# Kernel optimization log

Measured on AMD Instinct MI355X. Metric: run time of the kernel, lower is better.

The kernel has to match this reference:

```python
import jax, jax.numpy as jnp
import numpy as np

HIDDEN = 2048
N_HEADS = 32
HEAD_DIM = HIDDEN // N_HEADS  # 64
SEQ = 2048
BATCH = 1
CHUNK = 256
TOPK = 4
THETA = 10000.0
EPS = 1e-6
NEG = jnp.float32(-1e30)


def setup_inputs() -> dict:
    key = jax.random.key(0)
    ks = jax.random.split(key, 8)
    s = 0.02
    return {
        "hidden_states": jax.random.normal(ks[0], (BATCH, SEQ, HIDDEN), jnp.float32),
        "Wq": jax.random.normal(ks[1], (HIDDEN, HIDDEN), jnp.float32) * s,
        "Wk": jax.random.normal(ks[2], (HIDDEN, HIDDEN), jnp.float32) * s,
        "Wv": jax.random.normal(ks[3], (HIDDEN, HIDDEN), jnp.float32) * s,
        "Wo": jax.random.normal(ks[4], (HIDDEN, HIDDEN), jnp.float32) * s,
        "Wg1": jax.random.normal(ks[5], (HEAD_DIM, HIDDEN), jnp.float32) * s,
        "Wg2": jax.random.normal(ks[6], (HIDDEN, HEAD_DIM), jnp.float32) * s,
        "o_norm_weight": jnp.ones((HEAD_DIM,), jnp.float32),
    }


def _rope(t):
    # t: [B, S, H, D]; non-interleaved (NeoX-style) rotary over full head dim
    D = t.shape[-1]
    pos = jnp.arange(t.shape[1], dtype=jnp.float32)
    inv_freq = 1.0 / (THETA ** (jnp.arange(0, D, 2, dtype=jnp.float32) / D))
    freqs = pos[:, None] * inv_freq[None, :]            # [S, D/2]
    cos = jnp.cos(freqs)[None, :, None, :]
    sin = jnp.sin(freqs)[None, :, None, :]
    t1, t2 = t[..., : D // 2], t[..., D // 2:]
    return jnp.concatenate([t1 * cos - t2 * sin, t1 * sin + t2 * cos], axis=-1)


def reference(hidden_states, Wq, Wk, Wv, Wo, Wg1, Wg2, o_norm_weight):
    B, S, _ = hidden_states.shape
    H, D, C = N_HEADS, HEAD_DIM, CHUNK
    NC = S // C

    q = (hidden_states @ Wq.T).reshape(B, S, H, D)
    k = (hidden_states @ Wk.T).reshape(B, S, H, D)
    v = (hidden_states @ Wv.T).reshape(B, S, H, D)
    q, k = _rope(q), _rope(k)

    # --- MoBA gating: per-chunk mean-pooled keys scored against each query ---
    kmean = k.reshape(B, NC, C, H, D).mean(axis=2)           # [B, NC, H, D]
    gate = jnp.einsum('bshd,bnhd->bhsn', q, kmean)           # [B, H, S, NC]

    pos = jnp.arange(S)
    q_chunk = pos // C                                       # [S]
    chunk_ids = jnp.arange(NC)
    future = chunk_ids[None, :] > q_chunk[:, None]           # [S, NC]
    self_blk = chunk_ids[None, :] == q_chunk[:, None]
    gate = jnp.where(future[None, None], NEG, gate)
    gate = jnp.where(self_blk[None, None], -NEG, gate)       # self block always selected

    _, topk_idx = jax.lax.top_k(gate, TOPK)                  # [B, H, S, TOPK]
    sel = jax.nn.one_hot(topk_idx, NC, dtype=jnp.bool_).any(axis=-2)  # [B, H, S, NC]

    # --- block-sparse causal attention over selected chunks ---
    allowed = jnp.take(sel, q_chunk, axis=-1)                # [B, H, S, S] key j -> chunk j//C
    causal = pos[None, :] <= pos[:, None]                    # [S, S]
    allowed = allowed & causal[None, None]

    scale = 1.0 / np.sqrt(D)
    scores = jnp.einsum('bshd,bthd->bhst', q, k) * scale
    scores = jnp.where(allowed, scores, NEG)
    p = jax.nn.softmax(scores, axis=-1)
    o = jnp.einsum('bhst,bthd->bshd', p, v)                  # [B, S, H, D]

    # --- gated RMSNorm (FusedRMSNormGated, sigmoid activation) ---
    g = ((hidden_states @ Wg1.T) @ Wg2.T).reshape(B, S, H, D)
    rms = jax.lax.rsqrt(jnp.mean(o * o, axis=-1, keepdims=True) + EPS)
    o = o * rms * o_norm_weight * jax.nn.sigmoid(g)

    return (o.reshape(B, S, H * D)) @ Wo.T
```

## Files before the change

kernel.cpp:

```cpp
#include <hip/hip_runtime.h>
#include <hip/hip_bf16.h>


typedef __attribute__((ext_vector_type(8))) short s8v;
typedef __attribute__((ext_vector_type(4))) float f4v;

#define MFMA16(A,B,C) __builtin_amdgcn_mfma_f32_16x16x32_bf16(A,B,C,0,0,0)

__device__ __forceinline__ unsigned short f2b_rne(float f){
  unsigned u = __builtin_bit_cast(unsigned, f);
  u = (u + 0x7FFFu + ((u>>16)&1u)) >> 16;
  return (unsigned short)u;
}
__device__ __forceinline__ float b2f(unsigned short h){
  unsigned u = ((unsigned)h)<<16;
  return __builtin_bit_cast(float, u);
}
__device__ __forceinline__ unsigned pack2(float a, float b){
  return (unsigned)f2b_rne(a) | ((unsigned)f2b_rne(b)<<16);
}
__device__ __forceinline__ void gld16(const void* g, void* l){
  __builtin_amdgcn_global_load_lds((const __attribute__((address_space(1))) void*)g,
                                   (__attribute__((address_space(3))) void*)l, 16, 0, 0);
}

__global__ __launch_bounds__(256) void rtab_k(double2* __restrict__ tab){
  const int i = blockIdx.x*256 + threadIdx.x;
  if (i >= 2048*32) return;
  const int d2 = i & 31, s = i >> 5;
  const double invf = 1.0 / pow(10000.0, (double)d2 / 32.0);
  const double ph = (double)s * invf;
  tab[i] = make_double2(cos(ph), sin(ph));
}

__global__ __launch_bounds__(256) void f2b4_k(const float* __restrict__ s,
                                              unsigned short* __restrict__ d, int n4){
  int i = blockIdx.x*256 + threadIdx.x;
  if (i >= n4) return;
  const float4 v = *(const float4*)(s + (size_t)i*4);
  uint2 p; p.x = pack2(v.x, v.y); p.y = pack2(v.z, v.w);
  *(uint2*)(d + (size_t)i*4) = p;
}

__global__ __launch_bounds__(256) void f2bs_k(const float* __restrict__ s,
    unsigned short* __restrict__ hi, unsigned short* __restrict__ lo, int n4){
  int i = blockIdx.x*256 + threadIdx.x;
  if (i >= n4) return;
  const float4 v = *(const float4*)(s + (size_t)i*4);
  unsigned short h0 = f2b_rne(v.x), h1 = f2b_rne(v.y), h2 = f2b_rne(v.z), h3 = f2b_rne(v.w);
  uint2 ph; ph.x = (unsigned)h0 | ((unsigned)h1<<16); ph.y = (unsigned)h2 | ((unsigned)h3<<16);
  uint2 pl; pl.x = pack2(v.x - b2f(h0), v.y - b2f(h1));
  pl.y = pack2(v.z - b2f(h2), v.w - b2f(h3));
  *(uint2*)(hi + (size_t)i*4) = ph;
  *(uint2*)(lo + (size_t)i*4) = pl;
}

__global__ __launch_bounds__(1024) void wsum_k(const float* __restrict__ hs,
    const double2* __restrict__ tab, double* __restrict__ Ac, double* __restrict__ As){
  const int n = blockIdx.x, d2 = blockIdx.y, tid = threadIdx.x;
  double ac0=0, as0=0, ac1=0, as1=0;
  for (int i = 0; i < 256; ++i) {
    const int s = n*256 + i;
    const double2 t = tab[s*32 + d2];
    const double v0 = (double)hs[(size_t)s*2048 + tid];
    const double v1 = (double)hs[(size_t)s*2048 + tid + 1024];
    ac0 += t.x*v0; as0 += t.y*v0;
    ac1 += t.x*v1; as1 += t.y*v1;
  }
  const size_t ro = (size_t)(n*32 + d2)*2048;
  Ac[ro + tid]      = ac0*(1.0/256.0);
  Ac[ro + tid+1024] = ac1*(1.0/256.0);
  As[ro + tid]      = as0*(1.0/256.0);
  As[ro + tid+1024] = as1*(1.0/256.0);
}

__global__ __launch_bounds__(256) void transd_k(const double* __restrict__ in,
    double* __restrict__ out, int R, int C){
  __shared__ double t[64][65];
  const int c0 = blockIdx.x*64, r0 = blockIdx.y*64;
  const int tx = threadIdx.x & 63, ty4 = threadIdx.x >> 6;
  #pragma unroll
  for (int rr = 0; rr < 16; ++rr) {
    const int r = ty4*16 + rr;
    t[r][tx] = in[(size_t)(r0+r)*C + c0+tx];
  }
  __syncthreads();
  #pragma unroll
  for (int rr = 0; rr < 16; ++rr) {
    const int c = ty4*16 + rr;
    out[(size_t)(c0+c)*R + r0+tx] = t[tx][c];
  }
}

__global__ __launch_bounds__(256) void transf_k(const float* __restrict__ in,
    float* __restrict__ out, int R, int C){
  __shared__ float t[64][65];
  const int c0 = blockIdx.x*64, r0 = blockIdx.y*64;
  const int tx = threadIdx.x & 63, ty4 = threadIdx.x >> 6;
  #pragma unroll
  for (int rr = 0; rr < 16; ++rr) {
    const int r = ty4*16 + rr;
    t[r][tx] = in[(size_t)(r0+r)*C + c0+tx];
  }
  __syncthreads();
  #pragma unroll
  for (int rr = 0; rr < 16; ++rr) {
    const int c = ty4*16 + rr;
    out[(size_t)(c0+c)*R + r0+tx] = t[tx][c];
  }
}

__global__ __launch_bounds__(1024) void kmean2_k(const double* __restrict__ AcT,
    const double* __restrict__ AsT, const float* __restrict__ WkT,
    double* __restrict__ Km){
  const int n = blockIdx.x, h = blockIdx.y;
  const int tid = threadIdx.x, d = tid & 63, p = tid >> 6;
  const int d2 = d & 31;
  const bool hiHalf = d >= 32;
  double a = 0.0, b = 0.0;
  #pragma unroll 4
  for (int c = p*128; c < p*128 + 128; ++c) {
    const double x  = AcT[(size_t)c*256 + n*32 + d2];
    const double y  = AsT[(size_t)c*256 + n*32 + d2];
    const double w1 = (double)WkT[(size_t)c*2048 + h*64 + d2];
    const double w2 = (double)WkT[(size_t)c*2048 + h*64 + d2 + 32];
    if (!hiHalf) { a += x*w1; b += y*w2; }
    else         { a += y*w1; b += x*w2; }
  }
  __shared__ double red[1024];
  red[tid] = hiHalf ? (a + b) : (a - b);
  __syncthreads();
  if (p < 8) red[tid] += red[tid + 512];
  __syncthreads();
  if (p < 4) red[tid] += red[tid + 256];
  __syncthreads();
  if (p < 2) red[tid] += red[tid + 128];
  __syncthreads();
  if (p == 0)
    Km[(size_t)(n*32 + h)*64 + d] = red[d] + red[d + 64];
}

__global__ __launch_bounds__(256) void gate_topk_k(const float* __restrict__ Qf,
    const double* __restrict__ Km, unsigned char* __restrict__ Allow,
    unsigned char* __restrict__ Flags){
  const int h = blockIdx.x, c = blockIdx.y, t = threadIdx.x;
  __shared__ double km[512];
  km[t]     = Km[((t>>6)*32 + h)*64 + (t&63)];
  km[t+256] = Km[(((t+256)>>6)*32 + h)*64 + (t&63)];
  __syncthreads();
  const int s = c*256 + t;
  const float* qp = Qf + (size_t)s*2048 + h*64;
  double g[8] = {};
  for (int d = 0; d < 64; ++d) {
    const double qv = (double)qp[d];
    #pragma unroll
    for (int n2 = 0; n2 < 8; ++n2) g[n2] += qv*km[n2*64+d];
  }
  double margin = 1e300;
  if (c >= 4) {
    unsigned pm = 0;
    double v[4];
    for (int rep = 0; rep < 4; ++rep) {
      double best = -1e308; int bi = 0;
      #pragma unroll
      for (int n2 = 0; n2 < 8; ++n2) {
        const bool take = (n2 < c) && !((pm>>n2)&1u) && (g[n2] > best);
        best = take ? g[n2] : best;
        bi   = take ? n2 : bi;
      }
      v[rep] = best; pm |= 1u<<bi;
    }
    margin = v[2] - v[3];
  }
  Flags[h*2048 + s] = (margin < 1e-3) ? 1 : 0;
  #pragma unroll
  for (int n2 = 0; n2 < 8; ++n2) if (n2 > c) g[n2] = -1e300;
  g[c] = 1e300;
  unsigned mask = 0;
  for (int rep = 0; rep < 4; ++rep) {
    double best = -1e308; int bi = 0;
    #pragma unroll
    for (int n2 = 0; n2 < 8; ++n2) {
      const bool take = !((mask>>n2)&1u) && (g[n2] > best);
      best = take ? g[n2] : best;
      bi   = take ? n2 : bi;
    }
    mask |= 1u<<bi;
  }
  Allow[h*2048 + s] = (unsigned char)mask;
}

__global__ __launch_bounds__(64) void repair_k(
    const float* __restrict__ hs, const float* __restrict__ Wq,
    const double2* __restrict__ tab, const double* __restrict__ Km,
    const unsigned char* __restrict__ Flags, unsigned char* __restrict__ Allow)
{
  const int s = blockIdx.x, d = threadIdx.x;
  __shared__ double qr[64];
  __shared__ double g8[8];
  for (int h = 0; h < 32; ++h) {
    if (!Flags[h*2048 + s]) continue;
    const float* hrow = hs + (size_t)s*2048;
    const float* wrow = Wq + (size_t)(h*64 + d)*2048;
    double a0=0,a1=0,a2=0,a3=0;
    for (int k = 0; k < 2048; k += 4) {
      a0 += (double)hrow[k]  *(double)wrow[k];
      a1 += (double)hrow[k+1]*(double)wrow[k+1];
      a2 += (double)hrow[k+2]*(double)wrow[k+2];
      a3 += (double)hrow[k+3]*(double)wrow[k+3];
    }
    qr[d] = (a0+a1)+(a2+a3);
    __syncthreads();
    const double2 t = tab[s*32 + (d&31)];
    const double rot = (d < 32) ? (qr[d]*t.x - qr[d+32]*t.y)
                                : (qr[d-32]*t.y + qr[d]*t.x);
    __syncthreads();
    qr[d] = rot;
    __syncthreads();
    if (d < 8) {
      double g = 0;
      const double* kmp = Km + (size_t)(d*32 + h)*64;
      for (int dd = 0; dd < 64; ++dd) g += qr[dd]*kmp[dd];
      g8[d] = g;
    }
    __syncthreads();
    if (d == 0) {
      const int c = s >> 8;
      double g[8];
      #pragma unroll
      for (int n2 = 0; n2 < 8; ++n2)
        g[n2] = (n2 > c) ? -1e300 : ((n2 == c) ? 1e300 : g8[n2]);
      unsigned mask = 0;
      for (int rep = 0; rep < 4; ++rep) {
        double best = -1e308; int bi = 0;
        #pragma unroll
        for (int n2 = 0; n2 < 8; ++n2) {
          const bool take = !((mask>>n2)&1u) && (g[n2] > best);
          best = take ? g[n2] : best;
          bi   = take ? n2 : bi;
        }
        mask |= 1u<<bi;
      }
      Allow[h*2048 + s] = (unsigned char)mask;
    }
    __syncthreads();
  }
}

__global__ __launch_bounds__(256) void gemm4_bt(
    const unsigned short* __restrict__ Ah, const unsigned short* __restrict__ Al,
    const unsigned short* __restrict__ Bh, const unsigned short* __restrict__ Bl,
    float* __restrict__ C, int M, int N, int K)
{
  alignas(16) __shared__ char SAh[16384];
  alignas(16) __shared__ char SAl[16384];
  alignas(16) __shared__ char SBh[16384];
  alignas(16) __shared__ char SBl[16384];
  const int t = threadIdx.x;
  const int wave = t>>6, lane = t&63, lg = lane>>4, lr = lane&15;
  const int wm = wave >> 1, wn = wave & 1;
  const int m0 = blockIdx.x*128, n0 = blockIdx.y*128;
  const unsigned short* Ahb = Ah + (size_t)m0*K;
  const unsigned short* Alb = Al + (size_t)m0*K;
  const unsigned short* Bhb = Bh + (size_t)n0*K;
  const unsigned short* Blb = Bl + (size_t)n0*K;
  f4v acc[4][4] = {};
  #pragma unroll 1
  for (int kt = 0; kt < K; kt += 64) {
    __syncthreads();
    #pragma unroll
    for (int i = 0; i < 4; ++i) {
      const size_t go = (size_t)(i*32 + (t>>3))*K + kt + (t&7)*8;
      gld16(Ahb + go, SAh + i*4096 + wave*1024);
      gld16(Alb + go, SAl + i*4096 + wave*1024);
      gld16(Bhb + go, SBh + i*4096 + wave*1024);
      gld16(Blb + go, SBl + i*4096 + wave*1024);
    }
    __syncthreads();
    #pragma unroll
    for (int kk = 0; kk < 2; ++kk) {
      s8v ah[4], al[4], bh[4], bl[4];
      #pragma unroll
      for (int i = 0; i < 4; ++i) {
        const int ro = (wm*64 + i*16 + lr)*128 + kk*64 + lg*16;
        ah[i] = *(const s8v*)&SAh[ro];
        al[i] = *(const s8v*)&SAl[ro];
      }
      #pragma unroll
      for (int j = 0; j < 4; ++j) {
        const int ro = (wn*64 + j*16 + lr)*128 + kk*64 + lg*16;
        bh[j] = *(const s8v*)&SBh[ro];
        bl[j] = *(const s8v*)&SBl[ro];
      }
      #pragma unroll
      for (int i = 0; i < 4; ++i)
        #pragma unroll
        for (int j = 0; j < 4; ++j) {
          f4v a = acc[i][j];
          a = MFMA16(ah[i], bh[j], a);
          a = MFMA16(ah[i], bl[j], a);
          a = MFMA16(al[i], bh[j], a);
          a = MFMA16(al[i], bl[j], a);
          acc[i][j] = a;
        }
    }
  }
  #pragma unroll
  for (int i = 0; i < 4; ++i)
    #pragma unroll
    for (int j = 0; j < 4; ++j) {
      const int row = m0 + wm*64 + i*16 + lg*4;
      const int col = n0 + wn*64 + j*16 + lr;
      #pragma unroll
      for (int r = 0; r < 4; ++r)
        C[(size_t)(row+r)*N + col] = acc[i][j][r];
    }
}

template<int BM, int BN, int WN, bool OUTBF>
__global__ __launch_bounds__(256) void gemm_bt(
    const unsigned short* __restrict__ A, const unsigned short* __restrict__ B,
    void* __restrict__ C, int M, int N, int K)
{
  alignas(16) __shared__ char AsB[BM*128];
  alignas(16) __shared__ char BsB[BN*128];
  const int t = threadIdx.x;
  const int wave = t>>6, lane = t&63, lg = lane>>4, lr = lane&15;
  const int wm = wave / WN, wn = wave % WN;
  const int m0 = blockIdx.x*BM, n0 = blockIdx.y*BN;
  const unsigned short* Ab = A + (size_t)m0*K;
  const unsigned short* Bb = B + (size_t)n0*K;
  f4v acc[4][4] = {};
  #pragma unroll 1
  for (int kt = 0; kt < K; kt += 64) {
    __syncthreads();
    #pragma unroll
    for (int i = 0; i < BM/32; ++i)
      gld16(Ab + (size_t)(i*32 + (t>>3))*K + kt + (t&7)*8, AsB + i*4096 + wave*1024);
    #pragma unroll
    for (int i = 0; i < BN/32; ++i)
      gld16(Bb + (size_t)(i*32 + (t>>3))*K + kt + (t&7)*8, BsB + i*4096 + wave*1024);
    __syncthreads();
    #pragma unroll
    for (int kk = 0; kk < 2; ++kk) {
      s8v af[4], bfr[4];
      #pragma unroll
      for (int i = 0; i < 4; ++i)
        af[i] = *(const s8v*)&AsB[(wm*64 + i*16 + lr)*128 + kk*64 + lg*16];
      #pragma unroll
      for (int j = 0; j < 4; ++j)
        bfr[j] = *(const s8v*)&BsB[(wn*64 + j*16 + lr)*128 + kk*64 + lg*16];
      #pragma unroll
      for (int i = 0; i < 4; ++i)
        #pragma unroll
        for (int j = 0; j < 4; ++j)
          acc[i][j] = MFMA16(af[i], bfr[j], acc[i][j]);
    }
  }
  #pragma unroll
  for (int i = 0; i < 4; ++i)
    #pragma unroll
    for (int j = 0; j < 4; ++j) {
      const int row = m0 + wm*64 + i*16 + lg*4;
      const int col = n0 + wn*64 + j*16 + lr;
      #pragma unroll
      for (int r = 0; r < 4; ++r) {
        if (OUTBF) ((unsigned short*)C)[(size_t)(row+r)*N + col] = f2b_rne(acc[i][j][r]);
        else       ((float*)C)[(size_t)(row+r)*N + col] = acc[i][j][r];
      }
    }
}

__global__ __launch_bounds__(256) void rope32q_k(float* __restrict__ Qf,
    unsigned short* __restrict__ Qb, const double2* __restrict__ tab){
  const int idx = blockIdx.x*256 + threadIdx.x;
  const int d2 = idx & 31, hh = (idx>>5)&31, s = idx>>10;
  const double2 t = tab[s*32 + d2];
  const float cs = (float)t.x, sn = (float)t.y;
  const size_t base = (size_t)s*2048 + hh*64 + d2;
  const float q1 = Qf[base], q2 = Qf[base+32];
  const float o1 = q1*cs - q2*sn, o2 = q1*sn + q2*cs;
  Qf[base] = o1; Qf[base+32] = o2;
  Qb[base] = f2b_rne(o1); Qb[base+32] = f2b_rne(o2);
}

__global__ __launch_bounds__(256) void rope32_k(const float* __restrict__ Kf,
    unsigned short* __restrict__ Kb, const double2* __restrict__ tab){
  const int idx = blockIdx.x*256 + threadIdx.x;
  const int d2 = idx & 31, hh = (idx>>5)&31, s = idx>>10;
  const double2 t = tab[s*32 + d2];
  const float cs = (float)t.x, sn = (float)t.y;
  const size_t base = (size_t)s*2048 + hh*64 + d2;
  const float k1 = Kf[base], k2 = Kf[base+32];
  Kb[base]    = f2b_rne(k1*cs - k2*sn);
  Kb[base+32] = f2b_rne(k1*sn + k2*cs);
}

__global__ __launch_bounds__(256) void vtrans_k(const float* __restrict__ V,
                                                unsigned short* __restrict__ Vt){
  __shared__ unsigned short tile[64][68];
  const int s0 = blockIdx.x*64, c0 = blockIdx.y*64;
  const int tx = threadIdx.x & 63, ty = threadIdx.x >> 6;
  #pragma unroll
  for (int rr = 0; rr < 16; ++rr) {
    const int r = ty*16 + rr;
    tile[tx][r] = f2b_rne(V[(size_t)(s0+r)*2048 + c0+tx]);
  }
  __syncthreads();
  #pragma unroll
  for (int rr = 0; rr < 16; ++rr) {
    const int cc = ty*16 + rr;
    Vt[(size_t)(c0+cc)*2048 + s0+tx] = tile[cc][tx];
  }
}

__global__ __launch_bounds__(64) void attn_k(
    const unsigned short* __restrict__ Qb, const unsigned short* __restrict__ Kb,
    const unsigned short* __restrict__ Vt, const float* __restrict__ Gf,
    const unsigned char* __restrict__ Allow, const float* __restrict__ Wn,
    unsigned short* __restrict__ Ob)
{
  const int h = blockIdx.x, c = blockIdx.y, zb = blockIdx.z;
  const int lane = threadIdx.x, lg = lane>>4, lr = lane&15;
  const int qbase = c*256 + zb*16;
  alignas(16) __shared__ char P[2048];

  const size_t qrow = (size_t)(qbase + lr);
  const s8v qf0 = *(const s8v*)&Qb[qrow*2048 + h*64 + lg*8];
  const s8v qf1 = *(const s8v*)&Qb[qrow*2048 + h*64 + 32 + lg*8];
  const unsigned am = Allow[h*2048 + qrow];
  const int q = qbase + lr;
  const int sw = (lr&7)<<4;

  float mx = -1e30f, ls = 0.f;
  f4v ot[4] = {};

  for (int n = 0; n <= c; ++n) {
    if (!__ballot((am>>n)&1u)) continue;
    const int okc = (am>>n)&1;
    #pragma unroll 1
    for (int t4 = 0; t4 < 4; ++t4) {
      const int kb0 = n*256 + t4*64;
      s8v kf[4][2];
      #pragma unroll
      for (int i = 0; i < 4; ++i) {
        const size_t krow = (size_t)(kb0 + i*16 + lr);
        kf[i][0] = *(const s8v*)&Kb[krow*2048 + h*64 + lg*8];
        kf[i][1] = *(const s8v*)&Kb[krow*2048 + h*64 + 32 + lg*8];
      }
      f4v st[4];
      #pragma unroll
      for (int i = 0; i < 4; ++i) {
        f4v zz = {};
        zz = MFMA16(kf[i][0], qf0, zz);
        st[i] = MFMA16(kf[i][1], qf1, zz);
      }
      float cm = -__builtin_inff();
      #pragma unroll
      for (int i = 0; i < 4; ++i)
        #pragma unroll
        for (int r = 0; r < 4; ++r) {
          float v = st[i][r]*0.125f;
          const int key = kb0 + i*16 + lg*4 + r;
          const bool ok = okc && (n != c || key <= q);
          v = ok ? v : -__builtin_inff();
          st[i][r] = v;
          cm = fmaxf(cm, v);
        }
      cm = fmaxf(cm, __shfl_xor(cm, 16));
      cm = fmaxf(cm, __shfl_xor(cm, 32));
      const float nm = fmaxf(mx, cm);
      const float al = __expf(mx - nm);
      mx = nm;
      float ps = 0.f;
      #pragma unroll
      for (int i = 0; i < 4; ++i) {
        const float p0 = __expf(st[i][0]-mx);
        const float p1 = __expf(st[i][1]-mx);
        const float p2 = __expf(st[i][2]-mx);
        const float p3 = __expf(st[i][3]-mx);
        ps += (p0+p1)+(p2+p3);
        uint2 pk; pk.x = pack2(p0,p1); pk.y = pack2(p2,p3);
        *(uint2*)&P[lr*128 + ((i*32 + lg*8) ^ sw)] = pk;
      }
      ps += __shfl_xor(ps, 16);
      ps += __shfl_xor(ps, 32);
      ls = ls*al + ps;
      #pragma unroll
      for (int jd = 0; jd < 4; ++jd) ot[jd] *= al;
      asm volatile("s_waitcnt lgkmcnt(0)" ::: "memory");
      __builtin_amdgcn_sched_barrier(0);
      #pragma unroll
      for (int kk = 0; kk < 2; ++kk) {
        s8v vfr[4];
        #pragma unroll
        for (int jd = 0; jd < 4; ++jd)
          vfr[jd] = *(const s8v*)&Vt[(size_t)(h*64 + jd*16 + lr)*2048 + kb0 + kk*32 + lg*8];
        const s8v pfr = *(const s8v*)&P[lr*128 + ((kk*64 + lg*16) ^ sw)];
        #pragma unroll
        for (int jd = 0; jd < 4; ++jd)
          ot[jd] = MFMA16(vfr[jd], pfr, ot[jd]);
      }
      asm volatile("s_waitcnt lgkmcnt(0)" ::: "memory");
      __builtin_amdgcn_sched_barrier(0);
    }
  }
  const float inv_ = 1.0f/ls;
  float ssum = 0.f;
  #pragma unroll
  for (int jd = 0; jd < 4; ++jd)
    #pragma unroll
    for (int r = 0; r < 4; ++r) {
      const float o = ot[jd][r]*inv_;
      ot[jd][r] = o;
      ssum += o*o;
    }
  ssum += __shfl_xor(ssum, 16);
  ssum += __shfl_xor(ssum, 32);
  const float rmsv = rsqrtf(ssum*(1.0f/64.0f) + 1e-6f);
  #pragma unroll
  for (int jd = 0; jd < 4; ++jd) {
    const float4 w4 = *(const float4*)&Wn[jd*16 + lg*4];
    const float4 g4 = *(const float4*)&Gf[qrow*2048 + h*64 + jd*16 + lg*4];
    const float o0 = ot[jd][0]*rmsv*w4.x*(1.0f/(1.0f+__expf(-g4.x)));
    const float o1 = ot[jd][1]*rmsv*w4.y*(1.0f/(1.0f+__expf(-g4.y)));
    const float o2 = ot[jd][2]*rmsv*w4.z*(1.0f/(1.0f+__expf(-g4.z)));
    const float o3 = ot[jd][3]*rmsv*w4.w*(1.0f/(1.0f+__expf(-g4.w)));
    uint2 pk; pk.x = pack2(o0,o1); pk.y = pack2(o2,o3);
    *(uint2*)&Ob[qrow*2048 + h*64 + jd*16 + lg*4] = pk;
  }
}

extern "C" void kernel_launch(void* const* d_in, const int* in_sizes, int n_in,
                              void* d_out, int out_size, void* d_ws, size_t ws_size,
                              hipStream_t stream)
{
  const float* hs  = (const float*)d_in[0];
  const float* Wq  = (const float*)d_in[1];
  const float* Wk  = (const float*)d_in[2];
  const float* Wv  = (const float*)d_in[3];
  const float* Wo  = (const float*)d_in[4];
  const float* Wg1 = (const float*)d_in[5];
  const float* Wg2 = (const float*)d_in[6];
  const float* Wn  = (const float*)d_in[7];

  const size_t S2 = (size_t)2048*2048;
  const size_t MB = (size_t)1<<20;
  char* ws = (char*)d_ws;
  double2*        tab   = (double2*)       (ws);
  unsigned short* hsh   = (unsigned short*)(ws + 1*MB);
  unsigned short* hsl   = (unsigned short*)(ws + 9*MB);
  unsigned short* Wqh   = (unsigned short*)(ws + 17*MB);
  unsigned short* Wql   = (unsigned short*)(ws + 25*MB);
  unsigned short* Wkb   = (unsigned short*)(ws + 33*MB);
  unsigned short* Wvb   = (unsigned short*)(ws + 41*MB);
  unsigned short* Wg1b  = (unsigned short*)(ws + 49*MB);
  unsigned short* Wg2b  = (unsigned short*)(ws + 49*MB + 262144);
  unsigned short* g1b   = (unsigned short*)(ws + 49*MB + 524288);
  double*         km    = (double*)        (ws + 49*MB + 786432);
  unsigned char*  allow = (unsigned char*) (ws + 49*MB + 917504);
  unsigned char*  flags = (unsigned char*) (ws + 49*MB + 983040);
  float*          qf    = (float*)         (ws + 50*MB);
  float*          kf    = (float*)         (ws + 66*MB);
  float*          vf    = (float*)         (ws + 82*MB);
  double*         Ac    = (double*)        (ws + 98*MB);
  double*         As    = (double*)        (ws + 102*MB);
  unsigned short* kb    = (unsigned short*)(ws + 17*MB);
  unsigned short* qb    = (unsigned short*)(ws + 25*MB);
  double*         AcT   = (double*)        (ws + 33*MB);
  double*         AsT   = (double*)        (ws + 37*MB);
  float*          WkT   = (float*)         (ws + 66*MB);
  unsigned short* vt    = (unsigned short*)(ws + 66*MB);
  unsigned short* ob    = (unsigned short*)(ws + 74*MB);
  float*          gf    = (float*)         (ws + 82*MB);
  unsigned short* Wob   = (unsigned short*)(ws + 50*MB);
  (void)ws_size; (void)in_sizes; (void)n_in; (void)out_size;

  rtab_k<<<256,256,0,stream>>>(tab);
  f2bs_k<<<4096,256,0,stream>>>(hs, hsh, hsl, (int)(S2/4));
  f2bs_k<<<4096,256,0,stream>>>(Wq, Wqh, Wql, (int)(S2/4));
  f2b4_k<<<4096,256,0,stream>>>(Wk, Wkb, (int)(S2/4));
  f2b4_k<<<4096,256,0,stream>>>(Wv, Wvb, (int)(S2/4));
  f2b4_k<<<128,256,0,stream>>>(Wg1, Wg1b, 64*2048/4);
  f2b4_k<<<128,256,0,stream>>>(Wg2, Wg2b, 2048*64/4);

  gemm4_bt<<<dim3(16,16),256,0,stream>>>(hsh, hsl, Wqh, Wql, qf, 2048, 2048, 2048);
  gemm_bt<128,128,2,false><<<dim3(16,16),256,0,stream>>>(hsh, Wkb, kf, 2048, 2048, 2048);
  gemm_bt<128,128,2,false><<<dim3(16,16),256,0,stream>>>(hsh, Wvb, vf, 2048, 2048, 2048);

  rope32q_k<<<8192,256,0,stream>>>(qf, qb, tab);
  rope32_k<<<8192,256,0,stream>>>(kf, kb, tab);

  wsum_k<<<dim3(8,32),1024,0,stream>>>(hs, tab, Ac, As);
  transd_k<<<dim3(32,4),256,0,stream>>>(Ac, AcT, 256, 2048);
  transd_k<<<dim3(32,4),256,0,stream>>>(As, AsT, 256, 2048);
  transf_k<<<dim3(32,32),256,0,stream>>>(Wk, WkT, 2048, 2048);
  kmean2_k<<<dim3(8,32),1024,0,stream>>>(AcT, AsT, WkT, km);
  gate_topk_k<<<dim3(32,8),256,0,stream>>>(qf, km, allow, flags);
  repair_k<<<2048,64,0,stream>>>(hs, Wq, tab, km, flags, allow);

  vtrans_k<<<dim3(32,32),256,0,stream>>>(vf, vt);
  gemm_bt<256,64,1,true><<<dim3(8,1),256,0,stream>>>(hsh, Wg1b, g1b, 2048, 64, 2048);
  gemm_bt<128,128,2,false><<<dim3(16,16),256,0,stream>>>(g1b, Wg2b, gf, 2048, 2048, 64);

  attn_k<<<dim3(32,8,16),64,0,stream>>>(qb, kb, vt, gf, allow, Wn, ob);

  f2b4_k<<<4096,256,0,stream>>>(Wo, Wob, (int)(S2/4));
  gemm_bt<128,128,2,false><<<dim3(16,16),256,0,stream>>>(ob, Wob, d_out, 2048, 2048, 2048);
}
```

Baseline: 748.4 us.

## Fuse RoPE into Q/K GEMM epilogues and merge K/V projections into one launch

```diff
diff --git a/kernel.cpp b/kernel.cpp
--- a/kernel.cpp
+++ b/kernel.cpp
@@ -247,10 +247,11 @@
   }
 }
 
-__global__ __launch_bounds__(256) void gemm4_bt(
+__global__ __launch_bounds__(256) void gemm4q_k(
     const unsigned short* __restrict__ Ah, const unsigned short* __restrict__ Al,
     const unsigned short* __restrict__ Bh, const unsigned short* __restrict__ Bl,
-    float* __restrict__ C, int M, int N, int K)
+    const double2* __restrict__ tab,
+    float* __restrict__ Qf, unsigned short* __restrict__ Qb, int M, int N, int K)
 {
   alignas(16) __shared__ char SAh[16384];
   alignas(16) __shared__ char SAl[16384];
@@ -305,16 +306,100 @@
         }
     }
   }
+  const int colb = n0 + wn*64;
   #pragma unroll
   for (int i = 0; i < 4; ++i)
     #pragma unroll
-    for (int j = 0; j < 4; ++j) {
-      const int row = m0 + wm*64 + i*16 + lg*4;
-      const int col = n0 + wn*64 + j*16 + lr;
-      #pragma unroll
-      for (int r = 0; r < 4; ++r)
-        C[(size_t)(row+r)*N + col] = acc[i][j][r];
-    }
+    for (int jp = 0; jp < 2; ++jp) {
+      const int d2 = jp*16 + lr;
+      #pragma unroll
+      for (int r = 0; r < 4; ++r) {
+        const int row = m0 + wm*64 + i*16 + lg*4 + r;
+        const double2 tc = tab[row*32 + d2];
+        const float cs = (float)tc.x, sn = (float)tc.y;
+        const float q1 = acc[i][jp][r], q2 = acc[i][jp+2][r];
+        const float o1 = q1*cs - q2*sn, o2 = q1*sn + q2*cs;
+        const size_t base = (size_t)row*N + colb + d2;
+        Qf[base]      = o1;  Qf[base+32] = o2;
+        Qb[base]      = f2b_rne(o1);
+        Qb[base+32]   = f2b_rne(o2);
+      }
+    }
+}
+
+__global__ __launch_bounds__(256) void gemm_kv_k(
+    const unsigned short* __restrict__ A,
+    const unsigned short* __restrict__ Bk, const unsigned short* __restrict__ Bv,
+    const double2* __restrict__ tab,
+    unsigned short* __restrict__ Kb, unsigned short* __restrict__ Vb,
+    int M, int N, int K)
+{
+  alignas(16) __shared__ char AsB[16384];
+  alignas(16) __shared__ char BsB[16384];
+  const int z = blockIdx.z;
+  const unsigned short* B = z ? Bv : Bk;
+  const int t = threadIdx.x;
+  const int wave = t>>6, lane = t&63, lg = lane>>4, lr = lane&15;
+  const int wm = wave >> 1, wn = wave & 1;
+  const int m0 = blockIdx.x*128, n0 = blockIdx.y*128;
+  const unsigned short* Ab = A + (size_t)m0*K;
+  const unsigned short* Bb = B + (size_t)n0*K;
+  f4v acc[4][4] = {};
+  #pragma unroll 1
+  for (int kt = 0; kt < K; kt += 64) {
+    __syncthreads();
+    #pragma unroll
+    for (int i = 0; i < 4; ++i) {
+      gld16(Ab + (size_t)(i*32 + (t>>3))*K + kt + (t&7)*8, AsB + i*4096 + wave*1024);
+      gld16(Bb + (size_t)(i*32 + (t>>3))*K + kt + (t&7)*8, BsB + i*4096 + wave*1024);
+    }
+    __syncthreads();
+    #pragma unroll
+    for (int kk = 0; kk < 2; ++kk) {
+      s8v af[4], bfr[4];
+      #pragma unroll
+      for (int i = 0; i < 4; ++i)
+        af[i] = *(const s8v*)&AsB[(wm*64 + i*16 + lr)*128 + kk*64 + lg*16];
+      #pragma unroll
+      for (int j = 0; j < 4; ++j)
+        bfr[j] = *(const s8v*)&BsB[(wn*64 + j*16 + lr)*128 + kk*64 + lg*16];
+      #pragma unroll
+      for (int i = 0; i < 4; ++i)
+        #pragma unroll
+        for (int j = 0; j < 4; ++j)
+          acc[i][j] = MFMA16(af[i], bfr[j], acc[i][j]);
+    }
+  }
+  const int colb = n0 + wn*64;
+  if (z == 0) {
+    #pragma unroll
+    for (int i = 0; i < 4; ++i)
+      #pragma unroll
+      for (int jp = 0; jp < 2; ++jp) {
+        const int d2 = jp*16 + lr;
+        #pragma unroll
+        for (int r = 0; r < 4; ++r) {
+          const int row = m0 + wm*64 + i*16 + lg*4 + r;
+          const double2 tc = tab[row*32 + d2];
+          const float cs = (float)tc.x, sn = (float)tc.y;
+          const float k1 = acc[i][jp][r], k2 = acc[i][jp+2][r];
+          const size_t base = (size_t)row*N + colb + d2;
+          Kb[base]    = f2b_rne(k1*cs - k2*sn);
+          Kb[base+32] = f2b_rne(k1*sn + k2*cs);
+        }
+      }
+  } else {
+    #pragma unroll
+    for (int i = 0; i < 4; ++i)
+      #pragma unroll
+      for (int j = 0; j < 4; ++j) {
+        const int col = colb + j*16 + lr;
+        const int row0 = m0 + wm*64 + i*16 + lg*4;
+        #pragma unroll
+        for (int r = 0; r < 4; ++r)
+          Vb[(size_t)(row0+r)*N + col] = f2b_rne(acc[i][j][r]);
+      }
+  }
 }
 
 template<int BM, int BN, int WN, bool OUTBF>
@@ -371,32 +456,7 @@
     }
 }
 
-__global__ __launch_bounds__(256) void rope32q_k(float* __restrict__ Qf,
-    unsigned short* __restrict__ Qb, const double2* __restrict__ tab){
-  const int idx = blockIdx.x*256 + threadIdx.x;
-  const int d2 = idx & 31, hh = (idx>>5)&31, s = idx>>10;
-  const double2 t = tab[s*32 + d2];
-  const float cs = (float)t.x, sn = (float)t.y;
-  const size_t base = (size_t)s*2048 + hh*64 + d2;
-  const float q1 = Qf[base], q2 = Qf[base+32];
-  const float o1 = q1*cs - q2*sn, o2 = q1*sn + q2*cs;
-  Qf[base] = o1; Qf[base+32] = o2;
-  Qb[base] = f2b_rne(o1); Qb[base+32] = f2b_rne(o2);
-}
-
-__global__ __launch_bounds__(256) void rope32_k(const float* __restrict__ Kf,
-    unsigned short* __restrict__ Kb, const double2* __restrict__ tab){
-  const int idx = blockIdx.x*256 + threadIdx.x;
-  const int d2 = idx & 31, hh = (idx>>5)&31, s = idx>>10;
-  const double2 t = tab[s*32 + d2];
-  const float cs = (float)t.x, sn = (float)t.y;
-  const size_t base = (size_t)s*2048 + hh*64 + d2;
-  const float k1 = Kf[base], k2 = Kf[base+32];
-  Kb[base]    = f2b_rne(k1*cs - k2*sn);
-  Kb[base+32] = f2b_rne(k1*sn + k2*cs);
-}
-
-__global__ __launch_bounds__(256) void vtrans_k(const float* __restrict__ V,
+__global__ __launch_bounds__(256) void vtrans_k(const unsigned short* __restrict__ V,
                                                 unsigned short* __restrict__ Vt){
   __shared__ unsigned short tile[64][68];
   const int s0 = blockIdx.x*64, c0 = blockIdx.y*64;
@@ -404,7 +464,7 @@
   #pragma unroll
   for (int rr = 0; rr < 16; ++rr) {
     const int r = ty*16 + rr;
-    tile[tx][r] = f2b_rne(V[(size_t)(s0+r)*2048 + c0+tx]);
+    tile[tx][r] = V[(size_t)(s0+r)*2048 + c0+tx];
   }
   __syncthreads();
   #pragma unroll
@@ -561,12 +621,11 @@
   unsigned char*  allow = (unsigned char*) (ws + 49*MB + 917504);
   unsigned char*  flags = (unsigned char*) (ws + 49*MB + 983040);
   float*          qf    = (float*)         (ws + 50*MB);
-  float*          kf    = (float*)         (ws + 66*MB);
-  float*          vf    = (float*)         (ws + 82*MB);
+  unsigned short* vb    = (unsigned short*)(ws + 82*MB);
   double*         Ac    = (double*)        (ws + 98*MB);
   double*         As    = (double*)        (ws + 102*MB);
+  unsigned short* qb    = (unsigned short*)(ws + 106*MB);
   unsigned short* kb    = (unsigned short*)(ws + 17*MB);
-  unsigned short* qb    = (unsigned short*)(ws + 25*MB);
   double*         AcT   = (double*)        (ws + 33*MB);
   double*         AsT   = (double*)        (ws + 37*MB);
   float*          WkT   = (float*)         (ws + 66*MB);
@@ -584,12 +643,8 @@
   f2b4_k<<<128,256,0,stream>>>(Wg1, Wg1b, 64*2048/4);
   f2b4_k<<<128,256,0,stream>>>(Wg2, Wg2b, 2048*64/4);
 
-  gemm4_bt<<<dim3(16,16),256,0,stream>>>(hsh, hsl, Wqh, Wql, qf, 2048, 2048, 2048);
-  gemm_bt<128,128,2,false><<<dim3(16,16),256,0,stream>>>(hsh, Wkb, kf, 2048, 2048, 2048);
-  gemm_bt<128,128,2,false><<<dim3(16,16),256,0,stream>>>(hsh, Wvb, vf, 2048, 2048, 2048);
-
-  rope32q_k<<<8192,256,0,stream>>>(qf, qb, tab);
-  rope32_k<<<8192,256,0,stream>>>(kf, kb, tab);
+  gemm4q_k<<<dim3(16,16),256,0,stream>>>(hsh, hsl, Wqh, Wql, tab, qf, qb, 2048, 2048, 2048);
+  gemm_kv_k<<<dim3(16,16,2),256,0,stream>>>(hsh, Wkb, Wvb, tab, kb, vb, 2048, 2048, 2048);
 
   wsum_k<<<dim3(8,32),1024,0,stream>>>(hs, tab, Ac, As);
   transd_k<<<dim3(32,4),256,0,stream>>>(Ac, AcT, 256, 2048);
@@ -599,7 +654,7 @@
   gate_topk_k<<<dim3(32,8),256,0,stream>>>(qf, km, allow, flags);
   repair_k<<<2048,64,0,stream>>>(hs, Wq, tab, km, flags, allow);
 
-  vtrans_k<<<dim3(32,32),256,0,stream>>>(vf, vt);
+  vtrans_k<<<dim3(32,32),256,0,stream>>>(vb, vt);
   gemm_bt<256,64,1,true><<<dim3(8,1),256,0,stream>>>(hsh, Wg1b, g1b, 2048, 64, 2048);
   gemm_bt<128,128,2,false><<<dim3(16,16),256,0,stream>>>(g1b, Wg2b, gf, 2048, 2048, 64);
 
```

New measurement: 690.7 us (median of 2 runs). 1.08x faster.
